# Optimization experiments

Measured on AMD Instinct MI355X. Metric: run time of the kernel, lower is better.

## Reference

```python
import jax, jax.numpy as jnp
import numpy as np

GAMMA = 1.0 - 2.0 ** (-5)   # 0.96875, as in the module
NUM_GROUPS = 8
NUM_HEADS = 8
EPS = 1e-5


def setup_inputs() -> dict:
    key = jax.random.key(0)
    ks = jax.random.split(key, 8)
    M, S, Hd = 128, 512, 512  # num_segments, bonds per segment, hidden_size
    N = M * S
    return {
        "message": jax.random.normal(ks[0], (N, Hd), jnp.float32),
        "Wq": jax.random.normal(ks[1], (Hd, Hd), jnp.float32) / np.sqrt(Hd).astype(np.float32),
        "Wk": jax.random.normal(ks[2], (Hd, Hd), jnp.float32) / np.sqrt(Hd).astype(np.float32),
        "Wv": jax.random.normal(ks[3], (Hd, Hd), jnp.float32) / np.sqrt(Hd).astype(np.float32),
        "Wo": jax.random.normal(ks[4], (Hd, Hd), jnp.float32) / np.sqrt(Hd).astype(np.float32),
        "bo": jax.random.normal(ks[5], (Hd,), jnp.float32) * 0.01,
        "gn_w": jnp.ones((Hd,), jnp.float32),
        "gn_b": jnp.zeros((Hd,), jnp.float32),
        "num_segs": M,
        "seg_len": S,
    }


def _forward(message, Wq, Wk, Wv, Wo, bo, gn_w, gn_b, M, S):
    Hd = message.shape[1]
    H = NUM_HEADS
    d = Hd // H
    scale = jnp.float32(d ** (-0.5))
    gamma = jnp.float32(GAMMA)

    x = message.reshape(M, S, Hd)                       # equal contiguous segments
    q = (x @ Wq.T).reshape(M, S, H, d)
    k = (x @ Wk.T).reshape(M, S, H, d)
    v = (x @ Wv.T).reshape(M, S, H, d)

    # per-segment K^T V outer-product state contribution: [M, H, d, d]
    A = jnp.einsum('mshd,mshe->mhde', k, v)
    decay = gamma ** S  # gamma ** b_size for equal segments

    def step(r, a):
        # r = K_i^T V_i + gamma^{b_size} * r_prev  (state AFTER segment i, as in source)
        r_new = a + decay * r
        return r_new, r_new

    _, r_all = jax.lax.scan(step, jnp.zeros((H, d, d), x.dtype), A)  # [M, H, d, d]

    # intra-segment retention: (Q K^T) * scale @ V
    scores = jnp.einsum('mshd,mthd->mhst', q, k) * scale
    intra = jnp.einsum('mhst,mthd->mshd', scores, v)
    # cross/recurrent term: (Q @ r_i) * gamma^{i+1}  (note: NOT scaled by scale_factor)
    cross = jnp.einsum('mshd,mhde->mshe', q, r_all)
    g = (gamma ** jnp.arange(1, M + 1, dtype=jnp.float32))[:, None, None, None]
    h = jax.nn.relu(intra + cross * g)                  # activation; dropout p=0

    out = h.reshape(M, S, Hd) @ Wo.T + bo               # W_b_o
    res = x + out                                       # residual (dropout p=0)

    # GroupNorm(8, hidden): per segment (batch N=1), groups over hidden channels,
    # stats pooled over (hidden/8 group channels x S bonds)
    gsh = res.reshape(M, S, NUM_GROUPS, Hd // NUM_GROUPS)
    mean = gsh.mean(axis=(1, 3), keepdims=True)
    var = gsh.var(axis=(1, 3), keepdims=True)
    normed = ((gsh - mean) * jax.lax.rsqrt(var + EPS)).reshape(M, S, Hd)
    normed = normed * gn_w + gn_b

    flat = normed.reshape(M * S, Hd)
    # cached_zero_vector is prepended once before the first segment
    return jnp.concatenate([jnp.zeros((1, Hd), flat.dtype), flat], axis=0)


def reference(message, Wq, Wk, Wv, Wo, bo, gn_w, gn_b, num_segs, seg_len):
    return _forward(message, Wq, Wk, Wv, Wo, bo, gn_w, gn_b, num_segs, seg_len)
```

## Files before the change

kernel.cpp:

```cpp
#include <hip/hip_runtime.h>
#include <math.h>

#define M_SEG 128
#define S_SEG 512
#define HD 512
#define NHEAD 8
#define DHEAD 64
#define NROWS (M_SEG * S_SEG)
#define QKVLD 1536
#define GAMMA_F 0.96875f
#define SCALE_F 0.125f

typedef unsigned short u16;
typedef float f32x4 __attribute__((ext_vector_type(4)));
typedef __bf16 bf16x8 __attribute__((ext_vector_type(8)));
typedef unsigned short ushort8 __attribute__((ext_vector_type(8)));
typedef unsigned short ushort4v __attribute__((ext_vector_type(4)));

__device__ __forceinline__ u16 f2bf(float f) {
    union { float f; unsigned u; } x; x.f = f;
    unsigned r = x.u + 0x7FFFu + ((x.u >> 16) & 1u);
    return (u16)(r >> 16);
}
__device__ __forceinline__ float bf2f(u16 v) {
    union { unsigned u; float f; } x; x.u = ((unsigned)v) << 16;
    return x.f;
}

__device__ __forceinline__ void gload16(const u16* g, u16* l) {
    __builtin_amdgcn_global_load_lds(
        (const __attribute__((address_space(1))) void*)g,
        (__attribute__((address_space(3))) void*)l, 16, 0, 0);
}

__global__ __launch_bounds__(256) void convert_bf16(const float* __restrict__ in,
                                                    u16* __restrict__ outp, int n8)
{
    int idx = blockIdx.x * 256 + threadIdx.x;
    if (idx >= n8) return;
    const float4 a = *reinterpret_cast<const float4*>(&in[(size_t)idx * 8]);
    const float4 b = *reinterpret_cast<const float4*>(&in[(size_t)idx * 8 + 4]);
    ushort8 o;
    o[0] = f2bf(a.x); o[1] = f2bf(a.y); o[2] = f2bf(a.z); o[3] = f2bf(a.w);
    o[4] = f2bf(b.x); o[5] = f2bf(b.y); o[6] = f2bf(b.z); o[7] = f2bf(b.w);
    *reinterpret_cast<ushort8*>(&outp[(size_t)idx * 8]) = o;
}

__global__ __launch_bounds__(256) void convert_weights(const float* __restrict__ w0,
                                                       const float* __restrict__ w1,
                                                       const float* __restrict__ w2,
                                                       const float* __restrict__ w3,
                                                       u16* __restrict__ outp)
{
    const int which = blockIdx.y;
    const float* src = which == 0 ? w0 : which == 1 ? w1 : which == 2 ? w2 : w3;
    u16* dst = outp + (size_t)which * 262144;
    int idx = blockIdx.x * 256 + threadIdx.x;
    const float4 a = *reinterpret_cast<const float4*>(&src[(size_t)idx * 8]);
    const float4 b = *reinterpret_cast<const float4*>(&src[(size_t)idx * 8 + 4]);
    ushort8 o;
    o[0] = f2bf(a.x); o[1] = f2bf(a.y); o[2] = f2bf(a.z); o[3] = f2bf(a.w);
    o[4] = f2bf(b.x); o[5] = f2bf(b.y); o[6] = f2bf(b.z); o[7] = f2bf(b.w);
    *reinterpret_cast<ushort8*>(&dst[(size_t)idx * 8]) = o;
}

template<int EPI>
__global__ __launch_bounds__(512, 1) void gemm256(const u16* __restrict__ A, int lda,
                                                  const u16* __restrict__ B,
                                                  u16* __restrict__ Cv, int ldc, int ntile,
                                                  const u16* __restrict__ Xb,
                                                  const float* __restrict__ bias)
{
    __shared__ __align__(16) u16 sm[49152];
    const int t    = threadIdx.x;
    const int lane = t & 63;
    const int w    = t >> 6;
    const int wrow = w >> 2;
    const int wcol = w & 3;

    const int nwg  = gridDim.x;
    const int cpx  = nwg >> 3;
    const int bid  = blockIdx.x;
    const int sbid = (bid & 7) * cpx + (bid >> 3);
    const int mt = sbid / ntile, nt = sbid % ntile;
    const int rowBase = mt * 256, colBase = nt * 256;

    const int srow = t >> 2;
    const int scol = ((t & 3) ^ ((srow >> 1) & 3)) * 8;

    const size_t gA0 = (size_t)(rowBase +       srow) * lda + scol;
    const size_t gA1 = (size_t)(rowBase + 128 + srow) * lda + scol;
    const size_t gB0 = (size_t)(colBase +       srow) * HD  + scol;
    const size_t gB1 = (size_t)(colBase + 128 + srow) * HD  + scol;

    f32x4 acc[8][4];
#pragma unroll
    for (int i = 0; i < 8; ++i)
#pragma unroll
        for (int j = 0; j < 4; ++j)
            acc[i][j] = (f32x4){0.f, 0.f, 0.f, 0.f};

#define STAGE(kt, buf)                                                        \
    do {                                                                      \
        const int k0_ = (kt) * 32;                                            \
        u16* b_ = &sm[(buf) * 16384];                                         \
        gload16(&A[gA0 + k0_], &b_[        t * 8]);                           \
        gload16(&A[gA1 + k0_], &b_[4096  + t * 8]);                           \
        gload16(&B[gB0 + k0_], &b_[8192  + t * 8]);                           \
        gload16(&B[gB1 + k0_], &b_[12288 + t * 8]);                           \
    } while (0)

    STAGE(0, 0);
    STAGE(1, 1);

    const int frow = lane & 15;
    const int fkc  = lane >> 4;
    const int brow0 = (wcol & 1) * 64;

    for (int kt = 0; kt < 16; ++kt) {
        const int buf = kt % 3;
        if (kt + 2 < 16) STAGE(kt + 2, (kt + 2) % 3);
        if (kt < 14)       asm volatile("s_waitcnt vmcnt(8)" ::: "memory");
        else if (kt == 14) asm volatile("s_waitcnt vmcnt(4)" ::: "memory");
        else               asm volatile("s_waitcnt vmcnt(0)" ::: "memory");
        __builtin_amdgcn_s_barrier();
        __builtin_amdgcn_sched_barrier(0);

        const u16* Ah = &sm[buf * 16384 + wrow * 4096];
        const u16* Bh = &sm[buf * 16384 + 8192 + (wcol >> 1) * 4096];
        bf16x8 af[8], bfv[4];
#pragma unroll
        for (int mm = 0; mm < 8; ++mm) {
            const int r = mm * 16 + frow;
            af[mm] = *reinterpret_cast<const bf16x8*>(
                &Ah[r * 32 + ((fkc ^ ((r >> 1) & 3)) << 3)]);
        }
#pragma unroll
        for (int nn = 0; nn < 4; ++nn) {
            const int r = brow0 + nn * 16 + frow;
            bfv[nn] = *reinterpret_cast<const bf16x8*>(
                &Bh[r * 32 + ((fkc ^ ((r >> 1) & 3)) << 3)]);
        }
#pragma unroll
        for (int mm = 0; mm < 8; ++mm)
#pragma unroll
            for (int nn = 0; nn < 4; ++nn)
                acc[mm][nn] = __builtin_amdgcn_mfma_f32_16x16x32_bf16(af[mm], bfv[nn], acc[mm][nn], 0, 0, 0);

        __builtin_amdgcn_s_barrier();
    }
#undef STAGE

    const int orow = (lane >> 4) * 4;
    if (EPI == 0) {
        u16* ldsC = sm;
#pragma unroll
        for (int hp = 0; hp < 2; ++hp) {
            __syncthreads();
            if (wrow == hp) {
#pragma unroll
                for (int mm = 0; mm < 8; ++mm)
#pragma unroll
                    for (int nn = 0; nn < 4; ++nn) {
                        const int row0 = mm * 16 + orow;
                        const int col  = wcol * 64 + nn * 16 + frow;
#pragma unroll
                        for (int r = 0; r < 4; ++r)
                            ldsC[(row0 + r) * 256 + col] = f2bf(acc[mm][nn][r]);
                    }
            }
            __syncthreads();
#pragma unroll
            for (int p = 0; p < 8; ++p) {
                const int lin = p * 512 + t;
                const int row = lin >> 5, c8 = lin & 31;
                *reinterpret_cast<ushort8*>(
                    &Cv[(size_t)(rowBase + hp * 128 + row) * ldc + colBase + c8 * 8]) =
                    *reinterpret_cast<const ushort8*>(&ldsC[row * 256 + c8 * 8]);
            }
        }
    } else {
        float* ldsF = (float*)sm;
#pragma unroll
        for (int q = 0; q < 4; ++q) {
            __syncthreads();
            if (wrow == (q >> 1)) {
#pragma unroll
                for (int mm = 0; mm < 4; ++mm) {
                    const int macc = (q & 1) * 4 + mm;
#pragma unroll
                    for (int nn = 0; nn < 4; ++nn) {
                        const int row0 = mm * 16 + orow;
                        const int col  = wcol * 64 + nn * 16 + frow;
#pragma unroll
                        for (int r = 0; r < 4; ++r)
                            ldsF[(row0 + r) * 256 + col] = acc[macc][nn][r];
                    }
                }
            }
            __syncthreads();
#pragma unroll
            for (int p = 0; p < 8; ++p) {
                const int lin = p * 512 + t;
                const int row = lin >> 6, c4 = lin & 63;
                const int grow = rowBase + q * 64 + row;
                float4 a = *reinterpret_cast<const float4*>(&ldsF[row * 256 + c4 * 4]);
                ushort4v x4 = *reinterpret_cast<const ushort4v*>(
                    &Xb[(size_t)grow * HD + colBase + c4 * 4]);
                float4 b = *reinterpret_cast<const float4*>(&bias[colBase + c4 * 4]);
                ushort4v o;
                o[0] = f2bf(a.x + bf2f(x4[0]) + b.x);
                o[1] = f2bf(a.y + bf2f(x4[1]) + b.y);
                o[2] = f2bf(a.z + bf2f(x4[2]) + b.z);
                o[3] = f2bf(a.w + bf2f(x4[3]) + b.w);
                *reinterpret_cast<ushort4v*>(
                    &Cv[(size_t)grow * ldc + colBase + c4 * 4]) = o;
            }
        }
    }
}

__global__ __launch_bounds__(256) void kv_outer(const u16* __restrict__ qkv,
                                                float* __restrict__ Abuf)
{
    __shared__ float Ks[32][68];
    __shared__ float Vs[32][68];
    const int t  = threadIdx.x;
    const int hh = blockIdx.x;
    const int m  = blockIdx.y;
    const int td = (t >> 4) * 4;
    const int te = (t & 15) * 4;
    const int sl = t >> 3, cq = t & 7;
    float acc[4][4] = {};

    for (int s0 = 0; s0 < S_SEG; s0 += 32) {
        size_t g = (size_t)(m * S_SEG + s0 + sl) * QKVLD + hh * DHEAD + cq * 8;
        bf16x8 k8 = *reinterpret_cast<const bf16x8*>(&qkv[g + 512]);
        bf16x8 v8 = *reinterpret_cast<const bf16x8*>(&qkv[g + 1024]);
#pragma unroll
        for (int j = 0; j < 8; ++j) {
            Ks[sl][cq * 8 + j] = (float)k8[j];
            Vs[sl][cq * 8 + j] = (float)v8[j];
        }
        __syncthreads();
#pragma unroll
        for (int s = 0; s < 32; ++s) {
            float4 a4 = *reinterpret_cast<const float4*>(&Ks[s][td]);
            float4 b4 = *reinterpret_cast<const float4*>(&Vs[s][te]);
            float av[4] = {a4.x, a4.y, a4.z, a4.w};
            float bv[4] = {b4.x, b4.y, b4.z, b4.w};
#pragma unroll
            for (int i = 0; i < 4; ++i)
#pragma unroll
                for (int j = 0; j < 4; ++j)
                    acc[i][j] = fmaf(av[i], bv[j], acc[i][j]);
        }
        __syncthreads();
    }

#pragma unroll
    for (int i = 0; i < 4; ++i) {
        size_t base = ((size_t)(m * NHEAD + hh) * DHEAD + td + i) * DHEAD + te;
        *reinterpret_cast<float4*>(&Abuf[base]) = make_float4(acc[i][0], acc[i][1], acc[i][2], acc[i][3]);
    }
}

__global__ __launch_bounds__(256) void scan_kernel(const float* __restrict__ Abuf,
                                                   float* __restrict__ Bc)
{
    const int tid = blockIdx.x * 256 + threadIdx.x;
    const float decay = powf(GAMMA_F, (float)S_SEG);
    float r = 0.0f;
    float g = 1.0f;
    for (int m = 0; m < M_SEG; ++m) {
        float a = Abuf[(size_t)m * 32768 + tid];
        r = fmaf(decay, r, a);
        g *= GAMMA_F;
        Bc[(size_t)m * 32768 + tid] = fmaf(g, r, SCALE_F * a);
    }
}

__global__ __launch_bounds__(256) void h_mfma(u16* __restrict__ qkv,
                                              const float* __restrict__ Bc)
{
    __shared__ __align__(16) u16 BT[64 * 72];
    const int t    = threadIdx.x;
    const int lane = t & 63;
    const int w    = t >> 6;
    const int m    = blockIdx.y;
    const int sBase = blockIdx.x * 256 + w * 64;
    const int frow = lane & 15;
    const int fkc  = lane >> 4;

    for (int hh = 0; hh < NHEAD; ++hh) {
#pragma unroll
        for (int i = 0; i < 4; ++i) {
            int idx = t + i * 256;
            int d = idx >> 4, e4 = idx & 15;
            float4 v = *reinterpret_cast<const float4*>(
                &Bc[((size_t)(m * NHEAD + hh) * DHEAD + d) * DHEAD + e4 * 4]);
            BT[(e4 * 4 + 0) * 72 + d] = f2bf(v.x);
            BT[(e4 * 4 + 1) * 72 + d] = f2bf(v.y);
            BT[(e4 * 4 + 2) * 72 + d] = f2bf(v.z);
            BT[(e4 * 4 + 3) * 72 + d] = f2bf(v.w);
        }
        __syncthreads();

        f32x4 acc[4][4];
#pragma unroll
        for (int i = 0; i < 4; ++i)
#pragma unroll
            for (int j = 0; j < 4; ++j)
                acc[i][j] = (f32x4){0.f, 0.f, 0.f, 0.f};

#pragma unroll
        for (int ks = 0; ks < 2; ++ks) {
            bf16x8 af[4], bfr[4];
#pragma unroll
            for (int mm = 0; mm < 4; ++mm) {
                const int grow = m * S_SEG + sBase + mm * 16 + frow;
                af[mm] = *reinterpret_cast<const bf16x8*>(
                    &qkv[(size_t)grow * QKVLD + hh * DHEAD + ks * 32 + fkc * 8]);
                const int e = mm * 16 + frow;
                bfr[mm] = *reinterpret_cast<const bf16x8*>(&BT[e * 72 + ks * 32 + fkc * 8]);
            }
#pragma unroll
            for (int mm = 0; mm < 4; ++mm)
#pragma unroll
                for (int nn = 0; nn < 4; ++nn)
                    acc[mm][nn] = __builtin_amdgcn_mfma_f32_16x16x32_bf16(af[mm], bfr[nn], acc[mm][nn], 0, 0, 0);
        }

        const int orow = (lane >> 4) * 4;
#pragma unroll
        for (int mm = 0; mm < 4; ++mm)
#pragma unroll
            for (int nn = 0; nn < 4; ++nn) {
                const int col  = hh * DHEAD + nn * 16 + frow;
                const int row0 = m * S_SEG + sBase + mm * 16 + orow;
#pragma unroll
                for (int r = 0; r < 4; ++r)
                    qkv[(size_t)(row0 + r) * QKVLD + col] = f2bf(fmaxf(acc[mm][nn][r], 0.f));
            }
        __syncthreads();
    }
}

__global__ __launch_bounds__(256) void groupnorm_bf16(const u16* __restrict__ res,
                                                      float* __restrict__ out,
                                                      const float* __restrict__ gn_w,
                                                      const float* __restrict__ gn_b)
{
    const int g = blockIdx.x;
    const int m = blockIdx.y;
    const int t = threadIdx.x;
    const u16* base = res + (size_t)(m * S_SEG) * QKVLD + g * DHEAD;

    float sum = 0.0f, sq = 0.0f;
    for (int idx = t; idx < 4096; idx += 256) {
        int s = idx >> 3, c8 = idx & 7;
        ushort8 v = *reinterpret_cast<const ushort8*>(&base[(size_t)s * QKVLD + c8 * 8]);
#pragma unroll
        for (int j = 0; j < 8; ++j) {
            float f = bf2f(v[j]);
            sum += f; sq += f * f;
        }
    }
    __shared__ float rs[256], rq[256];
    rs[t] = sum; rq[t] = sq;
    __syncthreads();
    for (int off = 128; off > 0; off >>= 1) {
        if (t < off) { rs[t] += rs[t + off]; rq[t] += rq[t + off]; }
        __syncthreads();
    }
    __shared__ float smean, sinv;
    if (t == 0) {
        float mean = rs[0] * (1.0f / 32768.0f);
        float var  = rq[0] * (1.0f / 32768.0f) - mean * mean;
        smean = mean;
        sinv  = rsqrtf(var + 1e-5f);
    }
    __syncthreads();
    const float mean = smean, inv = sinv;

    for (int idx = t; idx < 4096; idx += 256) {
        int s = idx >> 3, c8 = idx & 7;
        ushort8 v = *reinterpret_cast<const ushort8*>(&base[(size_t)s * QKVLD + c8 * 8]);
        float o[8];
#pragma unroll
        for (int j = 0; j < 8; ++j) {
            float wj = gn_w[g * DHEAD + c8 * 8 + j];
            float bj = gn_b[g * DHEAD + c8 * 8 + j];
            o[j] = (bf2f(v[j]) - mean) * inv * wj + bj;
        }
        float* dst = &out[(size_t)(1 + m * S_SEG + s) * HD + g * DHEAD + c8 * 8];
        *reinterpret_cast<float4*>(dst)     = make_float4(o[0], o[1], o[2], o[3]);
        *reinterpret_cast<float4*>(dst + 4) = make_float4(o[4], o[5], o[6], o[7]);
    }
}

__global__ void zero_row(float* __restrict__ out)
{
    int i = blockIdx.x * 256 + threadIdx.x;
    if (i < HD) out[i] = 0.0f;
}

extern "C" void kernel_launch(void* const* d_in, const int* in_sizes, int n_in,
                              void* d_out, int out_size, void* d_ws, size_t ws_size,
                              hipStream_t stream)
{
    const float* msg = (const float*)d_in[0];
    const float* Wq  = (const float*)d_in[1];
    const float* Wk  = (const float*)d_in[2];
    const float* Wv  = (const float*)d_in[3];
    const float* Wo  = (const float*)d_in[4];
    const float* bo  = (const float*)d_in[5];
    const float* gnw = (const float*)d_in[6];
    const float* gnb = (const float*)d_in[7];
    float* out = (float*)d_out;

    u16*   msgb = (u16*)out;
    float* Abuf = out + 16777216;
    float* Bc   = out + 16777216 + 4194304;

    u16* Wb  = (u16*)d_ws;
    u16* qkv = Wb + 4 * 262144;
    u16* resB = qkv + 512;

    convert_weights<<<dim3(128, 4), 256, 0, stream>>>(Wq, Wk, Wv, Wo, Wb);
    convert_bf16<<<16384, 256, 0, stream>>>(msg, msgb, 4194304);

    gemm256<0><<<1536, 512, 0, stream>>>(msgb, HD, Wb, qkv, QKVLD, 6, nullptr, nullptr);

    kv_outer<<<dim3(NHEAD, M_SEG), 256, 0, stream>>>(qkv, Abuf);
    scan_kernel<<<128, 256, 0, stream>>>(Abuf, Bc);
    h_mfma<<<dim3(2, M_SEG), 256, 0, stream>>>(qkv, Bc);

    gemm256<1><<<512, 512, 0, stream>>>(qkv, QKVLD, Wb + 3 * 262144, resB, QKVLD, 2, msgb, bo);

    zero_row<<<2, 256, 0, stream>>>(out);
    groupnorm_bf16<<<dim3(8, M_SEG), 256, 0, stream>>>(resB, out, gnw, gnb);
}
```

Baseline: 397.9 us.

## Interleave GEMM tile loads with MFMA halves and retile kv_outer to single-wave blocks

The bf16 GEMM main loop now splits each k-step into two MFMA halves over the wave's rows. The next A tile is issued right after the barrier and the B tile between the two halves. The trailing barrier is dropped and s_setprio brackets the MFMA bursts, to overlap global-to-LDS copies with matrix work and cut sync overhead. Separately, kv_outer moves to 64-thread blocks with an 8x8 register tile per thread and vectorized LDS stores, which raises arithmetic intensity per LDS read but leaves fewer waves per block to hide latency.

```diff
diff --git a/kernel.cpp b/kernel.cpp
--- a/kernel.cpp
+++ b/kernel.cpp
@@ -65,11 +65,11 @@
 }
 
 template<int EPI>
-__global__ __launch_bounds__(512, 1) void gemm256(const u16* __restrict__ A, int lda,
-                                                  const u16* __restrict__ B,
-                                                  u16* __restrict__ Cv, int ldc, int ntile,
-                                                  const u16* __restrict__ Xb,
-                                                  const float* __restrict__ bias)
+__global__ __launch_bounds__(512, 1) void gemm8p(const u16* __restrict__ A, int lda,
+                                                 const u16* __restrict__ B,
+                                                 u16* __restrict__ Cv, int ldc, int ntile,
+                                                 const u16* __restrict__ Xb,
+                                                 const float* __restrict__ bias)
 {
     __shared__ __align__(16) u16 sm[49152];
     const int t    = threadIdx.x;
@@ -86,12 +86,11 @@
     const int rowBase = mt * 256, colBase = nt * 256;
 
     const int srow = t >> 2;
-    const int scol = ((t & 3) ^ ((srow >> 1) & 3)) * 8;
-
-    const size_t gA0 = (size_t)(rowBase +       srow) * lda + scol;
-    const size_t gA1 = (size_t)(rowBase + 128 + srow) * lda + scol;
-    const size_t gB0 = (size_t)(colBase +       srow) * HD  + scol;
-    const size_t gB1 = (size_t)(colBase + 128 + srow) * HD  + scol;
+    const int sks  = (t & 3) ^ ((srow >> 1) & 3);
+    const size_t gA0 = (size_t)(rowBase +       srow) * lda + sks * 8;
+    const size_t gA1 = (size_t)(rowBase + 128 + srow) * lda + sks * 8;
+    const size_t gB0 = (size_t)(colBase +       srow) * HD  + sks * 8;
+    const size_t gB1 = (size_t)(colBase + 128 + srow) * HD  + sks * 8;
 
     f32x4 acc[8][4];
 #pragma unroll
@@ -100,56 +99,71 @@
         for (int j = 0; j < 4; ++j)
             acc[i][j] = (f32x4){0.f, 0.f, 0.f, 0.f};
 
-#define STAGE(kt, buf)                                                        \
-    do {                                                                      \
-        const int k0_ = (kt) * 32;                                            \
-        u16* b_ = &sm[(buf) * 16384];                                         \
-        gload16(&A[gA0 + k0_], &b_[        t * 8]);                           \
-        gload16(&A[gA1 + k0_], &b_[4096  + t * 8]);                           \
-        gload16(&B[gB0 + k0_], &b_[8192  + t * 8]);                           \
-        gload16(&B[gB1 + k0_], &b_[12288 + t * 8]);                           \
+#define STAGE_A(kt, buf)                                                     \
+    do {                                                                     \
+        gload16(&A[gA0 + (kt) * 32], &sm[(buf) * 16384 + t * 8]);            \
+        gload16(&A[gA1 + (kt) * 32], &sm[(buf) * 16384 + 4096 + t * 8]);     \
     } while (0)
-
-    STAGE(0, 0);
-    STAGE(1, 1);
+#define STAGE_B(kt, buf)                                                     \
+    do {                                                                     \
+        gload16(&B[gB0 + (kt) * 32], &sm[(buf) * 16384 + 8192 + t * 8]);     \
+        gload16(&B[gB1 + (kt) * 32], &sm[(buf) * 16384 + 12288 + t * 8]);    \
+    } while (0)
+
+    STAGE_A(0, 0); STAGE_B(0, 0);
+    STAGE_A(1, 1); STAGE_B(1, 1);
 
     const int frow = lane & 15;
     const int fkc  = lane >> 4;
-    const int brow0 = (wcol & 1) * 64;
-
+
+#pragma unroll 1
     for (int kt = 0; kt < 16; ++kt) {
         const int buf = kt % 3;
-        if (kt + 2 < 16) STAGE(kt + 2, (kt + 2) % 3);
-        if (kt < 14)       asm volatile("s_waitcnt vmcnt(8)" ::: "memory");
-        else if (kt == 14) asm volatile("s_waitcnt vmcnt(4)" ::: "memory");
-        else               asm volatile("s_waitcnt vmcnt(0)" ::: "memory");
+        const int nbuf = (kt + 2) % 3;
+
+        if (kt < 15) asm volatile("s_waitcnt vmcnt(4)" ::: "memory");
+        else         asm volatile("s_waitcnt vmcnt(0)" ::: "memory");
         __builtin_amdgcn_s_barrier();
         __builtin_amdgcn_sched_barrier(0);
 
-        const u16* Ah = &sm[buf * 16384 + wrow * 4096];
-        const u16* Bh = &sm[buf * 16384 + 8192 + (wcol >> 1) * 4096];
-        bf16x8 af[8], bfv[4];
-#pragma unroll
-        for (int mm = 0; mm < 8; ++mm) {
-            const int r = mm * 16 + frow;
-            af[mm] = *reinterpret_cast<const bf16x8*>(
-                &Ah[r * 32 + ((fkc ^ ((r >> 1) & 3)) << 3)]);
+        if (kt < 14) STAGE_A(kt + 2, nbuf);
+        const u16* Ab = &sm[buf * 16384];
+        const u16* Bb = &sm[buf * 16384 + 8192];
+        bf16x8 af[4], bfv[4];
+#pragma unroll
+        for (int mf = 0; mf < 4; ++mf) {
+            const int r = wrow * 128 + mf * 16 + frow;
+            af[mf] = *reinterpret_cast<const bf16x8*>(&Ab[r * 32 + ((fkc ^ ((r >> 1) & 3)) << 3)]);
         }
 #pragma unroll
         for (int nn = 0; nn < 4; ++nn) {
-            const int r = brow0 + nn * 16 + frow;
-            bfv[nn] = *reinterpret_cast<const bf16x8*>(
-                &Bh[r * 32 + ((fkc ^ ((r >> 1) & 3)) << 3)]);
-        }
-#pragma unroll
-        for (int mm = 0; mm < 8; ++mm)
+            const int r = wcol * 64 + nn * 16 + frow;
+            bfv[nn] = *reinterpret_cast<const bf16x8*>(&Bb[r * 32 + ((fkc ^ ((r >> 1) & 3)) << 3)]);
+        }
+        __builtin_amdgcn_s_setprio(1);
+#pragma unroll
+        for (int mf = 0; mf < 4; ++mf)
 #pragma unroll
             for (int nn = 0; nn < 4; ++nn)
-                acc[mm][nn] = __builtin_amdgcn_mfma_f32_16x16x32_bf16(af[mm], bfv[nn], acc[mm][nn], 0, 0, 0);
-
-        __builtin_amdgcn_s_barrier();
-    }
-#undef STAGE
+                acc[mf][nn] = __builtin_amdgcn_mfma_f32_16x16x32_bf16(af[mf], bfv[nn], acc[mf][nn], 0, 0, 0);
+        __builtin_amdgcn_s_setprio(0);
+
+        if (kt < 14) STAGE_B(kt + 2, nbuf);
+#pragma unroll
+        for (int mf = 0; mf < 4; ++mf) {
+            const int r = wrow * 128 + 64 + mf * 16 + frow;
+            af[mf] = *reinterpret_cast<const bf16x8*>(&Ab[r * 32 + ((fkc ^ ((r >> 1) & 3)) << 3)]);
+        }
+        __builtin_amdgcn_s_setprio(1);
+#pragma unroll
+        for (int mf = 0; mf < 4; ++mf)
+#pragma unroll
+            for (int nn = 0; nn < 4; ++nn)
+                acc[4 + mf][nn] = __builtin_amdgcn_mfma_f32_16x16x32_bf16(af[mf], bfv[nn], acc[4 + mf][nn], 0, 0, 0);
+        __builtin_amdgcn_s_setprio(0);
+    }
+#undef STAGE_A
+#undef STAGE_B
 
     const int orow = (lane >> 4) * 4;
     if (EPI == 0) {
@@ -220,48 +234,58 @@
     }
 }
 
-__global__ __launch_bounds__(256) void kv_outer(const u16* __restrict__ qkv,
-                                                float* __restrict__ Abuf)
-{
-    __shared__ float Ks[32][68];
-    __shared__ float Vs[32][68];
+__global__ __launch_bounds__(64) void kv_outer(const u16* __restrict__ qkv,
+                                               float* __restrict__ Abuf)
+{
+    __shared__ __align__(16) float Ks[32][64];
+    __shared__ __align__(16) float Vs[32][64];
     const int t  = threadIdx.x;
     const int hh = blockIdx.x;
     const int m  = blockIdx.y;
-    const int td = (t >> 4) * 4;
-    const int te = (t & 15) * 4;
-    const int sl = t >> 3, cq = t & 7;
-    float acc[4][4] = {};
+    const int d0 = (t >> 3) * 8;
+    const int e0 = (t & 7) * 8;
+    float acc[8][8] = {};
 
     for (int s0 = 0; s0 < S_SEG; s0 += 32) {
-        size_t g = (size_t)(m * S_SEG + s0 + sl) * QKVLD + hh * DHEAD + cq * 8;
-        bf16x8 k8 = *reinterpret_cast<const bf16x8*>(&qkv[g + 512]);
-        bf16x8 v8 = *reinterpret_cast<const bf16x8*>(&qkv[g + 1024]);
-#pragma unroll
-        for (int j = 0; j < 8; ++j) {
-            Ks[sl][cq * 8 + j] = (float)k8[j];
-            Vs[sl][cq * 8 + j] = (float)v8[j];
+#pragma unroll
+        for (int i = 0; i < 4; ++i) {
+            const int slot = i * 64 + t;
+            const int s  = slot >> 3;
+            const int c8 = slot & 7;
+            size_t g = (size_t)(m * S_SEG + s0 + s) * QKVLD + hh * DHEAD + c8 * 8;
+            bf16x8 k8 = *reinterpret_cast<const bf16x8*>(&qkv[g + 512]);
+            bf16x8 v8 = *reinterpret_cast<const bf16x8*>(&qkv[g + 1024]);
+            float kf[8], vf[8];
+#pragma unroll
+            for (int j = 0; j < 8; ++j) { kf[j] = (float)k8[j]; vf[j] = (float)v8[j]; }
+            *reinterpret_cast<float4*>(&Ks[s][c8 * 8])     = make_float4(kf[0], kf[1], kf[2], kf[3]);
+            *reinterpret_cast<float4*>(&Ks[s][c8 * 8 + 4]) = make_float4(kf[4], kf[5], kf[6], kf[7]);
+            *reinterpret_cast<float4*>(&Vs[s][c8 * 8])     = make_float4(vf[0], vf[1], vf[2], vf[3]);
+            *reinterpret_cast<float4*>(&Vs[s][c8 * 8 + 4]) = make_float4(vf[4], vf[5], vf[6], vf[7]);
         }
         __syncthreads();
 #pragma unroll
         for (int s = 0; s < 32; ++s) {
-            float4 a4 = *reinterpret_cast<const float4*>(&Ks[s][td]);
-            float4 b4 = *reinterpret_cast<const float4*>(&Vs[s][te]);
-            float av[4] = {a4.x, a4.y, a4.z, a4.w};
-            float bv[4] = {b4.x, b4.y, b4.z, b4.w};
-#pragma unroll
-            for (int i = 0; i < 4; ++i)
-#pragma unroll
-                for (int j = 0; j < 4; ++j)
-                    acc[i][j] = fmaf(av[i], bv[j], acc[i][j]);
+            float4 ka = *reinterpret_cast<const float4*>(&Ks[s][d0]);
+            float4 kb = *reinterpret_cast<const float4*>(&Ks[s][d0 + 4]);
+            float4 va = *reinterpret_cast<const float4*>(&Vs[s][e0]);
+            float4 vb = *reinterpret_cast<const float4*>(&Vs[s][e0 + 4]);
+            float kv[8] = {ka.x, ka.y, ka.z, ka.w, kb.x, kb.y, kb.z, kb.w};
+            float vv[8] = {va.x, va.y, va.z, va.w, vb.x, vb.y, vb.z, vb.w};
+#pragma unroll
+            for (int i = 0; i < 8; ++i)
+#pragma unroll
+                for (int j = 0; j < 8; ++j)
+                    acc[i][j] = fmaf(kv[i], vv[j], acc[i][j]);
         }
         __syncthreads();
     }
 
 #pragma unroll
-    for (int i = 0; i < 4; ++i) {
-        size_t base = ((size_t)(m * NHEAD + hh) * DHEAD + td + i) * DHEAD + te;
-        *reinterpret_cast<float4*>(&Abuf[base]) = make_float4(acc[i][0], acc[i][1], acc[i][2], acc[i][3]);
+    for (int i = 0; i < 8; ++i) {
+        size_t base = ((size_t)(m * NHEAD + hh) * DHEAD + d0 + i) * DHEAD + e0;
+        *reinterpret_cast<float4*>(&Abuf[base])     = make_float4(acc[i][0], acc[i][1], acc[i][2], acc[i][3]);
+        *reinterpret_cast<float4*>(&Abuf[base + 4]) = make_float4(acc[i][4], acc[i][5], acc[i][6], acc[i][7]);
     }
 }
 
@@ -430,13 +454,13 @@
     convert_weights<<<dim3(128, 4), 256, 0, stream>>>(Wq, Wk, Wv, Wo, Wb);
     convert_bf16<<<16384, 256, 0, stream>>>(msg, msgb, 4194304);
 
-    gemm256<0><<<1536, 512, 0, stream>>>(msgb, HD, Wb, qkv, QKVLD, 6, nullptr, nullptr);
-
-    kv_outer<<<dim3(NHEAD, M_SEG), 256, 0, stream>>>(qkv, Abuf);
+    gemm8p<0><<<1536, 512, 0, stream>>>(msgb, HD, Wb, qkv, QKVLD, 6, nullptr, nullptr);
+
+    kv_outer<<<dim3(NHEAD, M_SEG), 64, 0, stream>>>(qkv, Abuf);
     scan_kernel<<<128, 256, 0, stream>>>(Abuf, Bc);
     h_mfma<<<dim3(2, M_SEG), 256, 0, stream>>>(qkv, Bc);
 
-    gemm256<1><<<512, 512, 0, stream>>>(qkv, QKVLD, Wb + 3 * 262144, resB, QKVLD, 2, msgb, bo);
+    gemm8p<1><<<512, 512, 0, stream>>>(qkv, QKVLD, Wb + 3 * 262144, resB, QKVLD, 2, msgb, bo);
 
     zero_row<<<2, 256, 0, stream>>>(out);
     groupnorm_bf16<<<dim3(8, M_SEG), 256, 0, stream>>>(resB, out, gnw, gnb);
```

Measured after the change: 418.3 us. 1.05x slower.

## Restructure GEMM into 8-phase ping-pong pipeline and use MFMA for KV outer products

Applied to the files above, without the earlier changes.

The 256x256 GEMM drops its 3-stage K=32 pipeline for K=64 double-buffered tiles staged in halves. Each K step runs eight quadrant MFMA phases, with global loads interleaved between them, barriers around each phase and setprio raised during MFMA. This aims to overlap memory traffic with tensor work. The per-segment K^T V outer product moves from scalar FP32 FMAs to bf16 MFMA, staging transposed K and V in swizzled shared memory. The cost is more barriers and larger shared-memory use in the GEMM.

```diff
diff --git a/kernel.cpp b/kernel.cpp
--- a/kernel.cpp
+++ b/kernel.cpp
@@ -65,18 +65,18 @@
 }
 
 template<int EPI>
-__global__ __launch_bounds__(512, 1) void gemm256(const u16* __restrict__ A, int lda,
-                                                  const u16* __restrict__ B,
-                                                  u16* __restrict__ Cv, int ldc, int ntile,
-                                                  const u16* __restrict__ Xb,
-                                                  const float* __restrict__ bias)
-{
-    __shared__ __align__(16) u16 sm[49152];
+__global__ __launch_bounds__(512, 1) void gemm8x(const u16* __restrict__ A, int lda,
+                                                 const u16* __restrict__ B,
+                                                 u16* __restrict__ Cv, int ldc, int ntile,
+                                                 const u16* __restrict__ Xb,
+                                                 const float* __restrict__ bias)
+{
+    __shared__ __align__(16) u16 sm[65536];
     const int t    = threadIdx.x;
     const int lane = t & 63;
     const int w    = t >> 6;
-    const int wrow = w >> 2;
-    const int wcol = w & 3;
+    const int wm   = w >> 2;
+    const int wn   = w & 3;
 
     const int nwg  = gridDim.x;
     const int cpx  = nwg >> 3;
@@ -85,13 +85,12 @@
     const int mt = sbid / ntile, nt = sbid % ntile;
     const int rowBase = mt * 256, colBase = nt * 256;
 
-    const int srow = t >> 2;
-    const int scol = ((t & 3) ^ ((srow >> 1) & 3)) * 8;
-
-    const size_t gA0 = (size_t)(rowBase +       srow) * lda + scol;
-    const size_t gA1 = (size_t)(rowBase + 128 + srow) * lda + scol;
-    const size_t gB0 = (size_t)(colBase +       srow) * HD  + scol;
-    const size_t gB1 = (size_t)(colBase + 128 + srow) * HD  + scol;
+    const int frow = lane & 15;
+    const int fkc  = lane >> 4;
+    const int orow = (lane >> 4) * 4;
+
+    const int r0  = t >> 3;
+    const int ksl = (t & 7) ^ (r0 & 7);
 
     f32x4 acc[8][4];
 #pragma unroll
@@ -100,70 +99,128 @@
         for (int j = 0; j < 4; ++j)
             acc[i][j] = (f32x4){0.f, 0.f, 0.f, 0.f};
 
-#define STAGE(kt, buf)                                                        \
-    do {                                                                      \
-        const int k0_ = (kt) * 32;                                            \
-        u16* b_ = &sm[(buf) * 16384];                                         \
-        gload16(&A[gA0 + k0_], &b_[        t * 8]);                           \
-        gload16(&A[gA1 + k0_], &b_[4096  + t * 8]);                           \
-        gload16(&B[gB0 + k0_], &b_[8192  + t * 8]);                           \
-        gload16(&B[gB1 + k0_], &b_[12288 + t * 8]);                           \
-    } while (0)
-
-    STAGE(0, 0);
-    STAGE(1, 1);
-
-    const int frow = lane & 15;
-    const int fkc  = lane >> 4;
-    const int brow0 = (wcol & 1) * 64;
-
-    for (int kt = 0; kt < 16; ++kt) {
-        const int buf = kt % 3;
-        if (kt + 2 < 16) STAGE(kt + 2, (kt + 2) % 3);
-        if (kt < 14)       asm volatile("s_waitcnt vmcnt(8)" ::: "memory");
-        else if (kt == 14) asm volatile("s_waitcnt vmcnt(4)" ::: "memory");
-        else               asm volatile("s_waitcnt vmcnt(0)" ::: "memory");
-        __builtin_amdgcn_s_barrier();
-        __builtin_amdgcn_sched_barrier(0);
-
-        const u16* Ah = &sm[buf * 16384 + wrow * 4096];
-        const u16* Bh = &sm[buf * 16384 + 8192 + (wcol >> 1) * 4096];
-        bf16x8 af[8], bfv[4];
-#pragma unroll
-        for (int mm = 0; mm < 8; ++mm) {
-            const int r = mm * 16 + frow;
-            af[mm] = *reinterpret_cast<const bf16x8*>(
-                &Ah[r * 32 + ((fkc ^ ((r >> 1) & 3)) << 3)]);
-        }
-#pragma unroll
-        for (int nn = 0; nn < 4; ++nn) {
-            const int r = brow0 + nn * 16 + frow;
-            bfv[nn] = *reinterpret_cast<const bf16x8*>(
-                &Bh[r * 32 + ((fkc ^ ((r >> 1) & 3)) << 3)]);
-        }
-#pragma unroll
-        for (int mm = 0; mm < 8; ++mm)
-#pragma unroll
-            for (int nn = 0; nn < 4; ++nn)
-                acc[mm][nn] = __builtin_amdgcn_mfma_f32_16x16x32_bf16(af[mm], bfv[nn], acc[mm][nn], 0, 0, 0);
-
-        __builtin_amdgcn_s_barrier();
-    }
-#undef STAGE
-
-    const int orow = (lane >> 4) * 4;
+#define STG(Mp, ld_, base_, kt, L, b, reg)                                    \
+    do {                                                                      \
+        u16* d_ = &sm[(b) * 32768 + (reg) * 16384 + (L) * 8192];              \
+        const u16* s_ = &Mp[(size_t)(base_ + (L) * 128 + r0) * (ld_)          \
+                            + (kt) * 64 + ksl * 8];                           \
+        gload16(s_, &d_[t * 8]);                                              \
+        gload16(s_ + (size_t)64 * (ld_), &d_[4096 + t * 8]);                  \
+    } while (0)
+#define STG_A(kt, L, b) STG(A, lda, rowBase, kt, L, b, 0)
+#define STG_B(kt, L, b) STG(B, HD, colBase, kt, L, b, 1)
+
+#define FRD_A(dst, b, mm0)                                                    \
+    do {                                                                      \
+        const u16* h_ = &sm[(b) * 32768 + wm * 8192];                         \
+        _Pragma("unroll")                                                     \
+        for (int q_ = 0; q_ < 4; ++q_)                                        \
+            _Pragma("unroll")                                                 \
+            for (int ks_ = 0; ks_ < 2; ++ks_) {                               \
+                const int row_ = ((mm0) + q_) * 16 + frow;                    \
+                const int sl_ = (ks_ * 4 + fkc) ^ (row_ & 7);                 \
+                dst[q_][ks_] = *reinterpret_cast<const bf16x8*>(              \
+                    &h_[row_ * 64 + sl_ * 8]);                                \
+            }                                                                 \
+    } while (0)
+#define FRD_B(dst, b, nn0)                                                    \
+    do {                                                                      \
+        const u16* h_ = &sm[(b) * 32768 + 16384 + (wn >> 1) * 8192];          \
+        _Pragma("unroll")                                                     \
+        for (int q_ = 0; q_ < 2; ++q_)                                        \
+            _Pragma("unroll")                                                 \
+            for (int ks_ = 0; ks_ < 2; ++ks_) {                               \
+                const int row_ = (wn & 1) * 64 + ((nn0) + q_) * 16 + frow;    \
+                const int sl_ = (ks_ * 4 + fkc) ^ (row_ & 7);                 \
+                dst[q_][ks_] = *reinterpret_cast<const bf16x8*>(              \
+                    &h_[row_ * 64 + sl_ * 8]);                                \
+            }                                                                 \
+    } while (0)
+#define MFQ(m0, n0, aA, bA)                                                   \
+    do {                                                                      \
+        __builtin_amdgcn_s_setprio(1);                                        \
+        _Pragma("unroll")                                                     \
+        for (int mm_ = 0; mm_ < 4; ++mm_)                                     \
+            _Pragma("unroll")                                                 \
+            for (int nn_ = 0; nn_ < 2; ++nn_)                                 \
+                _Pragma("unroll")                                             \
+                for (int ks_ = 0; ks_ < 2; ++ks_)                             \
+                    acc[(m0) + mm_][(n0) + nn_] =                             \
+                        __builtin_amdgcn_mfma_f32_16x16x32_bf16(              \
+                            aA[mm_][ks_], bA[nn_][ks_],                       \
+                            acc[(m0) + mm_][(n0) + nn_], 0, 0, 0);            \
+        __builtin_amdgcn_s_setprio(0);                                        \
+    } while (0)
+#define BARW()                                                                \
+    do {                                                                      \
+        __builtin_amdgcn_s_barrier();                                         \
+        asm volatile("s_waitcnt lgkmcnt(0)" ::: "memory");                    \
+        __builtin_amdgcn_sched_barrier(0);                                    \
+    } while (0)
+#define BAR() __builtin_amdgcn_s_barrier()
+
+    STG_A(0, 0, 0); STG_A(0, 1, 0); STG_B(0, 0, 0); STG_B(0, 1, 0);
+    STG_A(1, 0, 1);
+    asm volatile("s_waitcnt vmcnt(2)" ::: "memory");
+    BAR();
+
+    bf16x8 aL[4][2], aH[4][2], bLo[2][2], bHi[2][2];
+
+#pragma unroll 1
+    for (int j = 0; j < 4; ++j) {
+        const int te = 2 * j, to = 2 * j + 1;
+        FRD_A(aL, 0, 0); FRD_B(bLo, 0, 0);
+        STG_A(to, 1, 1);
+        BARW(); MFQ(0, 0, aL, bLo); BAR();
+        FRD_B(bHi, 0, 2);
+        STG_B(to, 0, 1);
+        BARW(); MFQ(0, 2, aL, bHi); BAR();
+        FRD_A(aH, 0, 4);
+        STG_B(to, 1, 1);
+        BARW(); MFQ(4, 0, aH, bLo); BAR();
+        if (j < 3) {
+            STG_A(te + 2, 0, 0);
+            asm volatile("s_waitcnt vmcnt(2)" ::: "memory");
+        } else {
+            asm volatile("s_waitcnt vmcnt(0)" ::: "memory");
+        }
+        BAR(); MFQ(4, 2, aH, bHi); BAR();
+        FRD_A(aL, 1, 0); FRD_B(bLo, 1, 0);
+        if (j < 3) STG_A(te + 2, 1, 0);
+        BARW(); MFQ(0, 0, aL, bLo); BAR();
+        FRD_B(bHi, 1, 2);
+        if (j < 3) STG_B(te + 2, 0, 0);
+        BARW(); MFQ(0, 2, aL, bHi); BAR();
+        FRD_A(aH, 1, 4);
+        if (j < 3) STG_B(te + 2, 1, 0);
+        BARW(); MFQ(4, 0, aH, bLo); BAR();
+        if (j < 3) {
+            STG_A(to + 2, 0, 1);
+            asm volatile("s_waitcnt vmcnt(2)" ::: "memory");
+        }
+        BAR(); MFQ(4, 2, aH, bHi); BAR();
+    }
+#undef STG
+#undef STG_A
+#undef STG_B
+#undef FRD_A
+#undef FRD_B
+#undef MFQ
+#undef BARW
+#undef BAR
+
     if (EPI == 0) {
         u16* ldsC = sm;
 #pragma unroll
         for (int hp = 0; hp < 2; ++hp) {
             __syncthreads();
-            if (wrow == hp) {
+            if (wm == hp) {
 #pragma unroll
                 for (int mm = 0; mm < 8; ++mm)
 #pragma unroll
                     for (int nn = 0; nn < 4; ++nn) {
                         const int row0 = mm * 16 + orow;
-                        const int col  = wcol * 64 + nn * 16 + frow;
+                        const int col  = wn * 64 + nn * 16 + frow;
 #pragma unroll
                         for (int r = 0; r < 4; ++r)
                             ldsC[(row0 + r) * 256 + col] = f2bf(acc[mm][nn][r]);
@@ -184,14 +241,14 @@
 #pragma unroll
         for (int q = 0; q < 4; ++q) {
             __syncthreads();
-            if (wrow == (q >> 1)) {
+            if (wm == (q >> 1)) {
 #pragma unroll
                 for (int mm = 0; mm < 4; ++mm) {
                     const int macc = (q & 1) * 4 + mm;
 #pragma unroll
                     for (int nn = 0; nn < 4; ++nn) {
                         const int row0 = mm * 16 + orow;
-                        const int col  = wcol * 64 + nn * 16 + frow;
+                        const int col  = wn * 64 + nn * 16 + frow;
 #pragma unroll
                         for (int r = 0; r < 4; ++r)
                             ldsF[(row0 + r) * 256 + col] = acc[macc][nn][r];
@@ -220,49 +277,89 @@
     }
 }
 
-__global__ __launch_bounds__(256) void kv_outer(const u16* __restrict__ qkv,
-                                                float* __restrict__ Abuf)
-{
-    __shared__ float Ks[32][68];
-    __shared__ float Vs[32][68];
-    const int t  = threadIdx.x;
-    const int hh = blockIdx.x;
-    const int m  = blockIdx.y;
-    const int td = (t >> 4) * 4;
-    const int te = (t & 15) * 4;
-    const int sl = t >> 3, cq = t & 7;
-    float acc[4][4] = {};
-
-    for (int s0 = 0; s0 < S_SEG; s0 += 32) {
-        size_t g = (size_t)(m * S_SEG + s0 + sl) * QKVLD + hh * DHEAD + cq * 8;
-        bf16x8 k8 = *reinterpret_cast<const bf16x8*>(&qkv[g + 512]);
-        bf16x8 v8 = *reinterpret_cast<const bf16x8*>(&qkv[g + 1024]);
-#pragma unroll
-        for (int j = 0; j < 8; ++j) {
-            Ks[sl][cq * 8 + j] = (float)k8[j];
-            Vs[sl][cq * 8 + j] = (float)v8[j];
-        }
-        __syncthreads();
-#pragma unroll
-        for (int s = 0; s < 32; ++s) {
-            float4 a4 = *reinterpret_cast<const float4*>(&Ks[s][td]);
-            float4 b4 = *reinterpret_cast<const float4*>(&Vs[s][te]);
-            float av[4] = {a4.x, a4.y, a4.z, a4.w};
-            float bv[4] = {b4.x, b4.y, b4.z, b4.w};
-#pragma unroll
-            for (int i = 0; i < 4; ++i)
-#pragma unroll
-                for (int j = 0; j < 4; ++j)
-                    acc[i][j] = fmaf(av[i], bv[j], acc[i][j]);
-        }
-        __syncthreads();
-    }
-
-#pragma unroll
-    for (int i = 0; i < 4; ++i) {
-        size_t base = ((size_t)(m * NHEAD + hh) * DHEAD + td + i) * DHEAD + te;
-        *reinterpret_cast<float4*>(&Abuf[base]) = make_float4(acc[i][0], acc[i][1], acc[i][2], acc[i][3]);
-    }
+__global__ __launch_bounds__(256) void kv_outer_mfma(const u16* __restrict__ qkv,
+                                                     float* __restrict__ Abuf)
+{
+    __shared__ __align__(16) u16 kT[2048];
+    __shared__ __align__(16) u16 vT[2048];
+    const int t    = threadIdx.x;
+    const int lane = t & 63;
+    const int w    = t >> 6;
+    const int hh   = blockIdx.x;
+    const int m    = blockIdx.y;
+    const int sl   = t & 31;
+    const int dg   = (t >> 5) * 8;
+    const int frow = lane & 15, fkc = lane >> 4, orow = (lane >> 4) * 4;
+    const size_t gbase = (size_t)(m * S_SEG) * QKVLD + 512 + hh * DHEAD + dg;
+
+    f32x4 acc[4];
+#pragma unroll
+    for (int i = 0; i < 4; ++i) acc[i] = (f32x4){0.f, 0.f, 0.f, 0.f};
+
+    ushort8 ka, va, kb, vb;
+
+#define LOADC(c, K8, V8)                                                      \
+    do {                                                                      \
+        size_t g_ = gbase + (size_t)((c) * 32 + sl) * QKVLD;                  \
+        K8 = *reinterpret_cast<const ushort8*>(&qkv[g_]);                     \
+        V8 = *reinterpret_cast<const ushort8*>(&qkv[g_ + 512]);               \
+    } while (0)
+#define WRTC(K8, V8)                                                          \
+    do {                                                                      \
+        _Pragma("unroll")                                                     \
+        for (int j = 0; j < 8; ++j) {                                         \
+            const int d_ = dg + j;                                            \
+            const int a_ = d_ * 32 + ((((sl >> 3) ^ ((d_ >> 1) & 3))) << 3) + (sl & 7); \
+            kT[a_] = K8[j];                                                   \
+            vT[a_] = V8[j];                                                   \
+        }                                                                     \
+    } while (0)
+#define CMPC()                                                                \
+    do {                                                                      \
+        bf16x8 kf[4], vf;                                                     \
+        _Pragma("unroll")                                                     \
+        for (int mf = 0; mf < 4; ++mf) {                                      \
+            const int d_ = mf * 16 + frow;                                    \
+            kf[mf] = *reinterpret_cast<const bf16x8*>(                        \
+                &kT[d_ * 32 + ((fkc ^ ((d_ >> 1) & 3)) << 3)]);               \
+        }                                                                     \
+        const int e_ = w * 16 + frow;                                         \
+        vf = *reinterpret_cast<const bf16x8*>(                                \
+            &vT[e_ * 32 + ((fkc ^ ((e_ >> 1) & 3)) << 3)]);                   \
+        _Pragma("unroll")                                                     \
+        for (int mf = 0; mf < 4; ++mf)                                        \
+            acc[mf] = __builtin_amdgcn_mfma_f32_16x16x32_bf16(kf[mf], vf, acc[mf], 0, 0, 0); \
+    } while (0)
+
+    LOADC(0, ka, va);
+#pragma unroll 1
+    for (int cc = 0; cc < 16; cc += 2) {
+        WRTC(ka, va);
+        LOADC(cc + 1, kb, vb);
+        asm volatile("s_waitcnt lgkmcnt(0)" ::: "memory");
+        __builtin_amdgcn_s_barrier();
+        __builtin_amdgcn_sched_barrier(0);
+        CMPC();
+        __builtin_amdgcn_s_barrier();
+
+        WRTC(kb, vb);
+        if (cc + 2 < 16) LOADC(cc + 2, ka, va);
+        asm volatile("s_waitcnt lgkmcnt(0)" ::: "memory");
+        __builtin_amdgcn_s_barrier();
+        __builtin_amdgcn_sched_barrier(0);
+        CMPC();
+        __builtin_amdgcn_s_barrier();
+    }
+#undef LOADC
+#undef WRTC
+#undef CMPC
+
+    const size_t hb = (size_t)(m * NHEAD + hh) * DHEAD * DHEAD;
+#pragma unroll
+    for (int mf = 0; mf < 4; ++mf)
+#pragma unroll
+        for (int r = 0; r < 4; ++r)
+            Abuf[hb + (size_t)(mf * 16 + orow + r) * DHEAD + w * 16 + frow] = acc[mf][r];
 }
 
 __global__ __launch_bounds__(256) void scan_kernel(const float* __restrict__ Abuf,
@@ -423,20 +520,20 @@
     float* Abuf = out + 16777216;
     float* Bc   = out + 16777216 + 4194304;
 
-    u16* Wb  = (u16*)d_ws;
-    u16* qkv = Wb + 4 * 262144;
+    u16* Wb   = (u16*)d_ws;
+    u16* qkv  = Wb + 4 * 262144;
     u16* resB = qkv + 512;
 
     convert_weights<<<dim3(128, 4), 256, 0, stream>>>(Wq, Wk, Wv, Wo, Wb);
     convert_bf16<<<16384, 256, 0, stream>>>(msg, msgb, 4194304);
 
-    gemm256<0><<<1536, 512, 0, stream>>>(msgb, HD, Wb, qkv, QKVLD, 6, nullptr, nullptr);
-
-    kv_outer<<<dim3(NHEAD, M_SEG), 256, 0, stream>>>(qkv, Abuf);
+    gemm8x<0><<<1536, 512, 0, stream>>>(msgb, HD, Wb, qkv, QKVLD, 6, nullptr, nullptr);
+
+    kv_outer_mfma<<<dim3(NHEAD, M_SEG), 256, 0, stream>>>(qkv, Abuf);
     scan_kernel<<<128, 256, 0, stream>>>(Abuf, Bc);
     h_mfma<<<dim3(2, M_SEG), 256, 0, stream>>>(qkv, Bc);
 
-    gemm256<1><<<512, 512, 0, stream>>>(qkv, QKVLD, Wb + 3 * 262144, resB, QKVLD, 2, msgb, bo);
+    gemm8x<1><<<512, 512, 0, stream>>>(qkv, QKVLD, Wb + 3 * 262144, resB, QKVLD, 2, msgb, bo);
 
     zero_row<<<2, 256, 0, stream>>>(out);
     groupnorm_bf16<<<dim3(8, M_SEG), 256, 0, stream>>>(resB, out, gnw, gnb);
```

New measurement: 367.2 us. 1.08x faster.
